# Kernel tuning notes

Hardware: AMD Instinct MI355X
Metric: run time of the kernel (lower is better)

## Reference

```python
import jax, jax.numpy as jnp
import numpy as np

N_NODES = 12288
N_EDGES = 393216
IN_FEAT = 2000
HID = 64


def setup_inputs() -> dict:
    key = jax.random.key(0)
    ks = jax.random.split(key, 8)
    features = jax.random.normal(ks[0], (N_NODES, IN_FEAT), dtype=jnp.float32)
    edge_weight = jax.random.uniform(ks[1], (N_EDGES, 1), dtype=jnp.float32)
    W1 = jax.random.normal(ks[2], (IN_FEAT, HID), dtype=jnp.float32) * 0.05
    b1 = jnp.zeros((HID,), dtype=jnp.float32)
    W2 = jax.random.normal(ks[3], (HID, HID), dtype=jnp.float32) * 0.05
    b2 = jnp.zeros((HID,), dtype=jnp.float32)
    src = jax.random.randint(ks[4], (N_EDGES,), 0, N_NODES, dtype=jnp.int32)
    dst = jax.random.randint(ks[5], (N_EDGES,), 0, N_NODES, dtype=jnp.int32)
    return {"features": features, "edge_weight": edge_weight, "W1": W1, "b1": b1,
            "W2": W2, "b2": b2, "src": src, "dst": dst}


def _weighted_graph_conv(x, W, b, src, dst, edge_weight, out_norm, in_norm):
    # norm='both': pre-scale by out_degree^-0.5
    h = x * out_norm[:, None]
    h = h @ W                                   # [N, out_feats]
    # gather -> per-edge weight multiply -> scatter-sum (DGL update_all)
    m = h[src] * edge_weight                    # [E, out_feats]
    agg = jax.ops.segment_sum(m, dst, num_segments=x.shape[0])
    # post-scale by in_degree^-0.5, add bias; activation=None
    return agg * in_norm[:, None] + b


def reference(features, edge_weight, W1, b1, W2, b2, src, dst):
    N = features.shape[0]
    ones = jnp.ones((src.shape[0],), dtype=jnp.float32)
    deg_out = jnp.clip(jax.ops.segment_sum(ones, src, num_segments=N), 1.0)
    deg_in = jnp.clip(jax.ops.segment_sum(ones, dst, num_segments=N), 1.0)
    out_norm = deg_out ** -0.5
    in_norm = deg_in ** -0.5
    x = _weighted_graph_conv(features, W1, b1, src, dst, edge_weight, out_norm, in_norm)
    x = _weighted_graph_conv(x, W2, b2, src, dst, edge_weight, out_norm, in_norm)
    # InnerProductDecoder with identity activation (dropout off / eval mode)
    adj_rec = x @ x.T                           # [N, N]
    return (adj_rec, x)
```

## Files before the change

kernel.cpp:

```cpp
#include <hip/hip_runtime.h>

#define N_NODES 12288
#define N_EDGES 393216
#define IN_FEAT 2000
#define HID 64
#define CAP 96

typedef __bf16 bf16x8 __attribute__((ext_vector_type(8)));
typedef float f32x16 __attribute__((ext_vector_type(16)));

__global__ void prep_kernel(const int* __restrict__ src,
                            float* __restrict__ deg_out,
                            const float* __restrict__ W1, unsigned int* __restrict__ Wpk) {
    int i = blockIdx.x * blockDim.x + threadIdx.x;
    if (i < IN_FEAT * HID) {
        float w = W1[i];
        __bf16 hb = (__bf16)w;
        __bf16 lb = (__bf16)(w - (float)hb);
        Wpk[i] = (unsigned int)__builtin_bit_cast(unsigned short, hb) |
                 ((unsigned int)__builtin_bit_cast(unsigned short, lb) << 16);
    }
    if (i < N_EDGES)
        atomicAdd(&deg_out[src[i]], 1.0f);
}

__global__ void fill_kernel(const int* __restrict__ dst, const int* __restrict__ src,
                            const float* __restrict__ ew, const float* __restrict__ deg_out,
                            int* __restrict__ cnt, int2* __restrict__ edata) {
    int e = blockIdx.x * blockDim.x + threadIdx.x;
    if (e < N_EDGES) {
        int s = src[e];
        int d = dst[e];
        int slot = atomicAdd(&cnt[d], 1);
        float wp = ew[e] / sqrtf(fmaxf(deg_out[s], 1.0f));
        edata[d * CAP + slot] = make_int2(s, __float_as_int(wp));
    }
}

__global__ __launch_bounds__(256) void gemm1_kernel(const float* __restrict__ A,
                                                    const unsigned int* __restrict__ Wpk,
                                                    float* __restrict__ h) {
    __shared__ __align__(16) char As[32768];
    int t = threadIdx.x;
    int w = t >> 6, l = t & 63, lr = l & 31, lh = l >> 5;
    int row0 = blockIdx.x * 64;
    int ksbase = blockIdx.y * 500;
    int col = (w >> 1) * 32 + lr;
    int lrow = (w & 1) * 32 + lr;
    const char* arow = As + lrow * 512;
    int rx = lr & 7;
    f32x16 acc = {};

    for (int tile = 0; tile < 4; ++tile) {
        int k0 = ksbase + tile * 128;
        int kvalid = (tile < 3) ? 128 : 116;
        __syncthreads();
#pragma unroll
        for (int i = 0; i < 8; ++i) {
            int c = t + i * 256;
            int r = c >> 5, u16 = c & 31;
            float4 v = make_float4(0.f, 0.f, 0.f, 0.f);
            if (u16 * 4 < kvalid)
                v = *(const float4*)&A[(size_t)(row0 + r) * IN_FEAT + k0 + u16 * 4];
            int uu = (u16 >> 1) ^ (r & 7);
            *(float4*)(As + r * 512 + uu * 32 + (u16 & 1) * 16) = v;
        }
        __syncthreads();

#pragma unroll
        for (int kk = 0; kk < 8; ++kk) {
            int uu = (kk * 2 + lh) ^ rx;
            float4 a01 = *(const float4*)(arow + uu * 32);
            float4 a23 = *(const float4*)(arow + uu * 32 + 16);
            float af[8] = {a01.x, a01.y, a01.z, a01.w, a23.x, a23.y, a23.z, a23.w};
            bf16x8 ah, al, wh, wl;
#pragma unroll
            for (int j = 0; j < 8; ++j) {
                float v = af[j];
                __bf16 hb = (__bf16)v;
                ah[j] = hb;
                al[j] = (__bf16)(v - (float)hb);
                int k = k0 + kk * 16 + lh * 8 + j;
                int kc = (k < IN_FEAT) ? k : 0;
                unsigned int wj = Wpk[kc * HID + col];
                wh[j] = __builtin_bit_cast(__bf16, (unsigned short)(wj & 0xffff));
                wl[j] = __builtin_bit_cast(__bf16, (unsigned short)(wj >> 16));
            }
            acc = __builtin_amdgcn_mfma_f32_32x32x16_bf16(ah, wh, acc, 0, 0, 0);
            acc = __builtin_amdgcn_mfma_f32_32x32x16_bf16(ah, wl, acc, 0, 0, 0);
            acc = __builtin_amdgcn_mfma_f32_32x32x16_bf16(al, wh, acc, 0, 0, 0);
        }
    }
#pragma unroll
    for (int r = 0; r < 16; ++r) {
        int orow = row0 + (w & 1) * 32 + (r & 3) + 8 * (r >> 2) + 4 * lh;
        atomicAdd(&h[orow * HID + col], acc[r]);
    }
}

__global__ __launch_bounds__(256) void layer1_kernel(const float* __restrict__ h,
                                                     const int2* __restrict__ edata,
                                                     const int* __restrict__ cnt,
                                                     const float* __restrict__ b1,
                                                     const float* __restrict__ W2,
                                                     float* __restrict__ h2) {
    __shared__ float Ws[64 * 64];
    __shared__ float xrow[4][64];
    int t = threadIdx.x;
#pragma unroll
    for (int i = 0; i < 16; ++i) Ws[t + i * 256] = W2[t + i * 256];

    int w = t >> 6;
    int n = blockIdx.x * 4 + w;
    int f = t & 63;
    float acc = 0.f;
    int beg = n * CAP, end = beg + cnt[n];
    int p = beg;
    for (; p + 4 <= end; p += 4) {
        int2 e0 = edata[p];
        int2 e1 = edata[p + 1];
        int2 e2 = edata[p + 2];
        int2 e3 = edata[p + 3];
        float h0 = h[(size_t)e0.x * HID + f];
        float h1 = h[(size_t)e1.x * HID + f];
        float h2v = h[(size_t)e2.x * HID + f];
        float h3 = h[(size_t)e3.x * HID + f];
        acc = fmaf(h0, __int_as_float(e0.y), acc);
        acc = fmaf(h1, __int_as_float(e1.y), acc);
        acc = fmaf(h2v, __int_as_float(e2.y), acc);
        acc = fmaf(h3, __int_as_float(e3.y), acc);
    }
    for (; p < end; ++p) {
        int2 e = edata[p];
        acc = fmaf(h[(size_t)e.x * HID + f], __int_as_float(e.y), acc);
    }
    float in_norm = rsqrtf(fmaxf((float)cnt[n], 1.0f));
    float x1 = acc * in_norm + b1[f];

    __syncthreads();
    xrow[w][f] = x1;
    float acc2 = 0.f;
#pragma unroll 16
    for (int k = 0; k < 64; ++k)
        acc2 = fmaf(xrow[w][k], Ws[k * 64 + f], acc2);
    h2[n * HID + f] = acc2;
}

__global__ __launch_bounds__(256) void gather2_kernel(const float* __restrict__ h,
                                                      const int2* __restrict__ edata,
                                                      const int* __restrict__ cnt,
                                                      const float* __restrict__ b2,
                                                      float* __restrict__ x_out,
                                                      __bf16* __restrict__ xh,
                                                      __bf16* __restrict__ xl) {
    int n = blockIdx.x * 4 + (threadIdx.x >> 6);
    int f = threadIdx.x & 63;
    float acc = 0.f;
    int beg = n * CAP, end = beg + cnt[n];
    int p = beg;
    for (; p + 4 <= end; p += 4) {
        int2 e0 = edata[p];
        int2 e1 = edata[p + 1];
        int2 e2 = edata[p + 2];
        int2 e3 = edata[p + 3];
        float h0 = h[(size_t)e0.x * HID + f];
        float h1 = h[(size_t)e1.x * HID + f];
        float h2 = h[(size_t)e2.x * HID + f];
        float h3 = h[(size_t)e3.x * HID + f];
        acc = fmaf(h0, __int_as_float(e0.y), acc);
        acc = fmaf(h1, __int_as_float(e1.y), acc);
        acc = fmaf(h2, __int_as_float(e2.y), acc);
        acc = fmaf(h3, __int_as_float(e3.y), acc);
    }
    for (; p < end; ++p) {
        int2 e = edata[p];
        acc = fmaf(h[(size_t)e.x * HID + f], __int_as_float(e.y), acc);
    }
    float in_norm = rsqrtf(fmaxf((float)cnt[n], 1.0f));
    float x = acc * in_norm + b2[f];
    int g = n * HID + f;
    x_out[g] = x;
    __bf16 hb = (__bf16)x;
    xh[g] = hb;
    xl[g] = (__bf16)(x - (float)hb);
}

__global__ __launch_bounds__(256) void adj_kernel(const __bf16* __restrict__ xh,
                                                  const __bf16* __restrict__ xl,
                                                  float* __restrict__ adj) {
    __shared__ __align__(16) char Bh[16384];
    __shared__ __align__(16) char Bl[16384];
    int t = threadIdx.x;
    int w = t >> 6, l = t & 63;
    int lr = l & 31, lh = l >> 5;
    int i0 = blockIdx.y * 128 + w * 32;
    int j0 = blockIdx.x * 128;

    const char* gh = (const char*)(xh + (size_t)j0 * HID);
    const char* gl = (const char*)(xl + (size_t)j0 * HID);
#pragma unroll
    for (int i = 0; i < 4; ++i) {
        int c = t + i * 256;
        int row = c >> 3, cin = c & 7;
        int dst = row * 128 + ((cin ^ (row & 7)) << 4);
        *(float4*)(Bh + dst) = *(const float4*)(gh + c * 16);
        *(float4*)(Bl + dst) = *(const float4*)(gl + c * 16);
    }

    const __bf16* arow_h = xh + (size_t)(i0 + lr) * HID + lh * 8;
    const __bf16* arow_l = xl + (size_t)(i0 + lr) * HID + lh * 8;
    bf16x8 ah[4], al[4];
#pragma unroll
    for (int kc = 0; kc < 4; ++kc) {
        ah[kc] = *(const bf16x8*)(arow_h + kc * 16);
        al[kc] = *(const bf16x8*)(arow_l + kc * 16);
    }
    __syncthreads();

#pragma unroll
    for (int ct = 0; ct < 4; ++ct) {
        int row = ct * 32 + lr;
        int rbase = row * 128, rxx = row & 7;
        bf16x8 bh[4], bl[4];
#pragma unroll
        for (int kc = 0; kc < 4; ++kc) {
            int off = rbase + (((kc * 2 + lh) ^ rxx) << 4);
            bh[kc] = *(const bf16x8*)(Bh + off);
            bl[kc] = *(const bf16x8*)(Bl + off);
        }
        f32x16 acc = {};
        acc = __builtin_amdgcn_mfma_f32_32x32x16_bf16(ah[0], bh[0], acc, 0, 0, 0);
        acc = __builtin_amdgcn_mfma_f32_32x32x16_bf16(ah[1], bh[1], acc, 0, 0, 0);
        acc = __builtin_amdgcn_mfma_f32_32x32x16_bf16(ah[2], bh[2], acc, 0, 0, 0);
        acc = __builtin_amdgcn_mfma_f32_32x32x16_bf16(ah[3], bh[3], acc, 0, 0, 0);
        acc = __builtin_amdgcn_mfma_f32_32x32x16_bf16(ah[0], bl[0], acc, 0, 0, 0);
        acc = __builtin_amdgcn_mfma_f32_32x32x16_bf16(ah[1], bl[1], acc, 0, 0, 0);
        acc = __builtin_amdgcn_mfma_f32_32x32x16_bf16(ah[2], bl[2], acc, 0, 0, 0);
        acc = __builtin_amdgcn_mfma_f32_32x32x16_bf16(ah[3], bl[3], acc, 0, 0, 0);
        acc = __builtin_amdgcn_mfma_f32_32x32x16_bf16(al[0], bh[0], acc, 0, 0, 0);
        acc = __builtin_amdgcn_mfma_f32_32x32x16_bf16(al[1], bh[1], acc, 0, 0, 0);
        acc = __builtin_amdgcn_mfma_f32_32x32x16_bf16(al[2], bh[2], acc, 0, 0, 0);
        acc = __builtin_amdgcn_mfma_f32_32x32x16_bf16(al[3], bh[3], acc, 0, 0, 0);

#pragma unroll
        for (int r = 0; r < 16; ++r) {
            int rrow = (r & 3) + 8 * (r >> 2) + 4 * lh;
            adj[(size_t)(i0 + rrow) * N_NODES + j0 + ct * 32 + lr] = acc[r];
        }
    }
}

extern "C" void kernel_launch(void* const* d_in, const int* in_sizes, int n_in,
                              void* d_out, int out_size, void* d_ws, size_t ws_size,
                              hipStream_t stream) {
    const float* features = (const float*)d_in[0];
    const float* ew       = (const float*)d_in[1];
    const float* W1       = (const float*)d_in[2];
    const float* b1       = (const float*)d_in[3];
    const float* W2       = (const float*)d_in[4];
    const float* b2       = (const float*)d_in[5];
    const int*   src      = (const int*)d_in[6];
    const int*   dst      = (const int*)d_in[7];

    float* out   = (float*)d_out;
    float* x_out = out + (size_t)N_NODES * N_NODES;

    const size_t NH = (size_t)N_NODES * HID;
    float* ws      = (float*)d_ws;
    float* deg_out = ws;
    int*   cnt     = (int*)(ws + N_NODES);
    float* h       = ws + 2 * N_NODES;
    int2*  edata   = (int2*)(h + NH);
    unsigned int* Wpk = (unsigned int*)(edata + (size_t)N_NODES * CAP);
    float* h2      = (float*)(Wpk + IN_FEAT * HID + 2);
    __bf16* xh     = (__bf16*)(h2 + NH);
    __bf16* xl     = xh + NH;

    hipMemsetAsync(ws, 0, (size_t)(2 * N_NODES + NH) * sizeof(float), stream);

    prep_kernel<<<N_EDGES / 256, 256, 0, stream>>>(src, deg_out, W1, Wpk);
    fill_kernel<<<N_EDGES / 256, 256, 0, stream>>>(dst, src, ew, deg_out, cnt, edata);

    gemm1_kernel<<<dim3(N_NODES / 64, 4), 256, 0, stream>>>(features, Wpk, h);

    layer1_kernel<<<N_NODES / 4, 256, 0, stream>>>(h, edata, cnt, b1, W2, h2);

    gather2_kernel<<<N_NODES / 4, 256, 0, stream>>>(h2, edata, cnt, b2, x_out, xh, xl);

    adj_kernel<<<dim3(N_NODES / 128, N_NODES / 128), 256, 0, stream>>>(xh, xl, out);
}
```

Before: 257.0 us.

## Fuse degree/CSR fill and GEMM1 into one launch, defer out-norm to gather

Merges the degree count, edge bucketing and first GEMM into a single kernel: 768 blocks run the GEMM and the rest fill the edge lists, so the two phases can overlap and two launches go away. The W1 bf16 hi/lo split is now done inline in the GEMM instead of a prep pass. Because deg_out is no longer final when edges are written, the out-degree normalisation moves into the gather kernels, which now do an extra deg_out load and rsqrt per edge. The fused edge blocks use 32KB of LDS they never touch, which may limit occupancy.

```diff
diff --git a/kernel.cpp b/kernel.cpp
--- a/kernel.cpp
+++ b/kernel.cpp
@@ -9,42 +9,29 @@
 typedef __bf16 bf16x8 __attribute__((ext_vector_type(8)));
 typedef float f32x16 __attribute__((ext_vector_type(16)));
 
-__global__ void prep_kernel(const int* __restrict__ src,
-                            float* __restrict__ deg_out,
-                            const float* __restrict__ W1, unsigned int* __restrict__ Wpk) {
-    int i = blockIdx.x * blockDim.x + threadIdx.x;
-    if (i < IN_FEAT * HID) {
-        float w = W1[i];
-        __bf16 hb = (__bf16)w;
-        __bf16 lb = (__bf16)(w - (float)hb);
-        Wpk[i] = (unsigned int)__builtin_bit_cast(unsigned short, hb) |
-                 ((unsigned int)__builtin_bit_cast(unsigned short, lb) << 16);
-    }
-    if (i < N_EDGES)
-        atomicAdd(&deg_out[src[i]], 1.0f);
-}
-
-__global__ void fill_kernel(const int* __restrict__ dst, const int* __restrict__ src,
-                            const float* __restrict__ ew, const float* __restrict__ deg_out,
-                            int* __restrict__ cnt, int2* __restrict__ edata) {
-    int e = blockIdx.x * blockDim.x + threadIdx.x;
-    if (e < N_EDGES) {
-        int s = src[e];
-        int d = dst[e];
+__global__ __launch_bounds__(256) void work_kernel(const float* __restrict__ A,
+                                                   const float* __restrict__ W1,
+                                                   float* __restrict__ h,
+                                                   const int* __restrict__ dst,
+                                                   const int* __restrict__ src,
+                                                   const float* __restrict__ ew,
+                                                   float* __restrict__ deg_out,
+                                                   int* __restrict__ cnt,
+                                                   int2* __restrict__ edata) {
+    __shared__ __align__(16) char As[32768];
+    int bx = blockIdx.x;
+    if (bx >= 768) {
+        int e = (bx - 768) * 256 + threadIdx.x;
+        int s = src[e], d = dst[e];
+        atomicAdd(&deg_out[s], 1.0f);
         int slot = atomicAdd(&cnt[d], 1);
-        float wp = ew[e] / sqrtf(fmaxf(deg_out[s], 1.0f));
-        edata[d * CAP + slot] = make_int2(s, __float_as_int(wp));
-    }
-}
-
-__global__ __launch_bounds__(256) void gemm1_kernel(const float* __restrict__ A,
-                                                    const unsigned int* __restrict__ Wpk,
-                                                    float* __restrict__ h) {
-    __shared__ __align__(16) char As[32768];
+        edata[d * CAP + slot] = make_int2(s, __float_as_int(ew[e]));
+        return;
+    }
     int t = threadIdx.x;
     int w = t >> 6, l = t & 63, lr = l & 31, lh = l >> 5;
-    int row0 = blockIdx.x * 64;
-    int ksbase = blockIdx.y * 500;
+    int row0 = (bx >> 2) * 64;
+    int ksbase = (bx & 3) * 500;
     int col = (w >> 1) * 32 + lr;
     int lrow = (w & 1) * 32 + lr;
     const char* arow = As + lrow * 512;
@@ -82,9 +69,10 @@
                 al[j] = (__bf16)(v - (float)hb);
                 int k = k0 + kk * 16 + lh * 8 + j;
                 int kc = (k < IN_FEAT) ? k : 0;
-                unsigned int wj = Wpk[kc * HID + col];
-                wh[j] = __builtin_bit_cast(__bf16, (unsigned short)(wj & 0xffff));
-                wl[j] = __builtin_bit_cast(__bf16, (unsigned short)(wj >> 16));
+                float wv = W1[kc * HID + col];
+                __bf16 wb = (__bf16)wv;
+                wh[j] = wb;
+                wl[j] = (__bf16)(wv - (float)wb);
             }
             acc = __builtin_amdgcn_mfma_f32_32x32x16_bf16(ah, wh, acc, 0, 0, 0);
             acc = __builtin_amdgcn_mfma_f32_32x32x16_bf16(ah, wl, acc, 0, 0, 0);
@@ -101,6 +89,7 @@
 __global__ __launch_bounds__(256) void layer1_kernel(const float* __restrict__ h,
                                                      const int2* __restrict__ edata,
                                                      const int* __restrict__ cnt,
+                                                     const float* __restrict__ deg_out,
                                                      const float* __restrict__ b1,
                                                      const float* __restrict__ W2,
                                                      float* __restrict__ h2) {
@@ -121,18 +110,23 @@
         int2 e1 = edata[p + 1];
         int2 e2 = edata[p + 2];
         int2 e3 = edata[p + 3];
+        float o0 = rsqrtf(fmaxf(deg_out[e0.x], 1.0f));
+        float o1 = rsqrtf(fmaxf(deg_out[e1.x], 1.0f));
+        float o2 = rsqrtf(fmaxf(deg_out[e2.x], 1.0f));
+        float o3 = rsqrtf(fmaxf(deg_out[e3.x], 1.0f));
         float h0 = h[(size_t)e0.x * HID + f];
         float h1 = h[(size_t)e1.x * HID + f];
         float h2v = h[(size_t)e2.x * HID + f];
         float h3 = h[(size_t)e3.x * HID + f];
-        acc = fmaf(h0, __int_as_float(e0.y), acc);
-        acc = fmaf(h1, __int_as_float(e1.y), acc);
-        acc = fmaf(h2v, __int_as_float(e2.y), acc);
-        acc = fmaf(h3, __int_as_float(e3.y), acc);
+        acc = fmaf(h0, __int_as_float(e0.y) * o0, acc);
+        acc = fmaf(h1, __int_as_float(e1.y) * o1, acc);
+        acc = fmaf(h2v, __int_as_float(e2.y) * o2, acc);
+        acc = fmaf(h3, __int_as_float(e3.y) * o3, acc);
     }
     for (; p < end; ++p) {
         int2 e = edata[p];
-        acc = fmaf(h[(size_t)e.x * HID + f], __int_as_float(e.y), acc);
+        float o = rsqrtf(fmaxf(deg_out[e.x], 1.0f));
+        acc = fmaf(h[(size_t)e.x * HID + f], __int_as_float(e.y) * o, acc);
     }
     float in_norm = rsqrtf(fmaxf((float)cnt[n], 1.0f));
     float x1 = acc * in_norm + b1[f];
@@ -149,6 +143,7 @@
 __global__ __launch_bounds__(256) void gather2_kernel(const float* __restrict__ h,
                                                       const int2* __restrict__ edata,
                                                       const int* __restrict__ cnt,
+                                                      const float* __restrict__ deg_out,
                                                       const float* __restrict__ b2,
                                                       float* __restrict__ x_out,
                                                       __bf16* __restrict__ xh,
@@ -163,18 +158,23 @@
         int2 e1 = edata[p + 1];
         int2 e2 = edata[p + 2];
         int2 e3 = edata[p + 3];
+        float o0 = rsqrtf(fmaxf(deg_out[e0.x], 1.0f));
+        float o1 = rsqrtf(fmaxf(deg_out[e1.x], 1.0f));
+        float o2 = rsqrtf(fmaxf(deg_out[e2.x], 1.0f));
+        float o3 = rsqrtf(fmaxf(deg_out[e3.x], 1.0f));
         float h0 = h[(size_t)e0.x * HID + f];
         float h1 = h[(size_t)e1.x * HID + f];
         float h2 = h[(size_t)e2.x * HID + f];
         float h3 = h[(size_t)e3.x * HID + f];
-        acc = fmaf(h0, __int_as_float(e0.y), acc);
-        acc = fmaf(h1, __int_as_float(e1.y), acc);
-        acc = fmaf(h2, __int_as_float(e2.y), acc);
-        acc = fmaf(h3, __int_as_float(e3.y), acc);
+        acc = fmaf(h0, __int_as_float(e0.y) * o0, acc);
+        acc = fmaf(h1, __int_as_float(e1.y) * o1, acc);
+        acc = fmaf(h2, __int_as_float(e2.y) * o2, acc);
+        acc = fmaf(h3, __int_as_float(e3.y) * o3, acc);
     }
     for (; p < end; ++p) {
         int2 e = edata[p];
-        acc = fmaf(h[(size_t)e.x * HID + f], __int_as_float(e.y), acc);
+        float o = rsqrtf(fmaxf(deg_out[e.x], 1.0f));
+        acc = fmaf(h[(size_t)e.x * HID + f], __int_as_float(e.y) * o, acc);
     }
     float in_norm = rsqrtf(fmaxf((float)cnt[n], 1.0f));
     float x = acc * in_norm + b2[f];
@@ -271,21 +271,18 @@
     int*   cnt     = (int*)(ws + N_NODES);
     float* h       = ws + 2 * N_NODES;
     int2*  edata   = (int2*)(h + NH);
-    unsigned int* Wpk = (unsigned int*)(edata + (size_t)N_NODES * CAP);
-    float* h2      = (float*)(Wpk + IN_FEAT * HID + 2);
+    float* h2      = (float*)(edata + (size_t)N_NODES * CAP);
     __bf16* xh     = (__bf16*)(h2 + NH);
     __bf16* xl     = xh + NH;
 
     hipMemsetAsync(ws, 0, (size_t)(2 * N_NODES + NH) * sizeof(float), stream);
 
-    prep_kernel<<<N_EDGES / 256, 256, 0, stream>>>(src, deg_out, W1, Wpk);
-    fill_kernel<<<N_EDGES / 256, 256, 0, stream>>>(dst, src, ew, deg_out, cnt, edata);
-
-    gemm1_kernel<<<dim3(N_NODES / 64, 4), 256, 0, stream>>>(features, Wpk, h);
-
-    layer1_kernel<<<N_NODES / 4, 256, 0, stream>>>(h, edata, cnt, b1, W2, h2);
-
-    gather2_kernel<<<N_NODES / 4, 256, 0, stream>>>(h2, edata, cnt, b2, x_out, xh, xl);
+    work_kernel<<<768 + N_EDGES / 256, 256, 0, stream>>>(features, W1, h,
+                                                         dst, src, ew, deg_out, cnt, edata);
+
+    layer1_kernel<<<N_NODES / 4, 256, 0, stream>>>(h, edata, cnt, deg_out, b1, W2, h2);
+
+    gather2_kernel<<<N_NODES / 4, 256, 0, stream>>>(h2, edata, cnt, deg_out, b2, x_out, xh, xl);
 
     adj_kernel<<<dim3(N_NODES / 128, N_NODES / 128), 256, 0, stream>>>(xh, xl, out);
 }
```

After: 248.0 us. 3.5% less time.
